# Kernel tuning notes

Measured on AMD Instinct MI355X. Metric: run time of the kernel, lower is better.

The kernel has to match this reference:

```python
import jax, jax.numpy as jnp
import numpy as np

N_NODES = 100000
N_EDGES = 3200000
D_IN = 128
D_OUT = 128


def setup_inputs() -> dict:
    key = jax.random.key(0)
    k1, k2, k3, k4, k5, k6 = jax.random.split(key, 6)
    x = jax.random.normal(k1, (N_NODES, D_IN), dtype=jnp.float32)
    edge_row = jnp.sort(jax.random.randint(k2, (N_EDGES,), 0, N_NODES, dtype=jnp.int32))
    edge_col = jax.random.randint(k3, (N_EDGES,), 0, N_NODES, dtype=jnp.int32)
    edge_val = jax.random.uniform(k4, (N_EDGES,), dtype=jnp.float32)
    stdv = 1.0 / np.sqrt(D_OUT)
    weight = jax.random.uniform(k5, (D_IN, D_OUT), dtype=jnp.float32, minval=-stdv, maxval=stdv)
    bias = jax.random.uniform(k6, (D_OUT,), dtype=jnp.float32, minval=-stdv, maxval=stdv)
    return {"x": x, "edge_row": edge_row, "edge_col": edge_col,
            "edge_val": edge_val, "weight": weight, "bias": bias}


def reference(x, edge_row, edge_col, edge_val, weight, bias):
    # support = A @ x  (sparse COO SpMM via gather + segment-sum scatter)
    gathered = x[edge_col] * edge_val[:, None]          # [E, D_IN]
    support = jax.ops.segment_sum(gathered, edge_row, num_segments=N_NODES)  # [N, D_IN]
    # output = support @ W + b
    return support @ weight + bias
```

## Files before the change

kernel.cpp:

```cpp
#include <hip/hip_runtime.h>

#define NNODES 100000
#define NEDGES 3200000
#define DIM    128

typedef __bf16  bf16x8 __attribute__((ext_vector_type(8)));
typedef unsigned short u16;
typedef u16     u16x8  __attribute__((ext_vector_type(8)));
typedef float   f32x4  __attribute__((ext_vector_type(4)));
typedef float   f32x2  __attribute__((ext_vector_type(2)));

__device__ __forceinline__ u16 f2bf(float f) {
    union { float f; unsigned int i; } c;
    c.f = f;
    unsigned int x = c.i;
    unsigned int rounding = 0x7fff + ((x >> 16) & 1);
    x += rounding;
    return (u16)(x >> 16);
}

__device__ __forceinline__ float bf2f(u16 u) {
    union { unsigned int i; float f; } c;
    c.i = ((unsigned int)u) << 16;
    return c.f;
}

__device__ __forceinline__ bf16x8 ldfrag_bf(const u16* p) {
    u16x8 u = *(const u16x8*)p;
    return __builtin_bit_cast(bf16x8, u);
}

__device__ __forceinline__ bf16x8 ldfrag_f32(const float* p) {
    f32x4 a = *(const f32x4*)p;
    f32x4 b = *(const f32x4*)(p + 4);
    u16x8 u;
#pragma unroll
    for (int i = 0; i < 4; ++i) u[i] = f2bf(a[i]);
#pragma unroll
    for (int i = 0; i < 4; ++i) u[4 + i] = f2bf(b[i]);
    return __builtin_bit_cast(bf16x8, u);
}

__global__ void build_row_ptr(const int* __restrict__ edge_row,
                              int* __restrict__ row_ptr) {
    int n = blockIdx.x * blockDim.x + threadIdx.x;
    if (n > NNODES) return;
    int lo = 0, hi = NEDGES;
    while (lo < hi) {
        int mid = (lo + hi) >> 1;
        if (edge_row[mid] < n) lo = mid + 1; else hi = mid;
    }
    row_ptr[n] = lo;
}

__global__ void prep_wt(const float* __restrict__ w, u16* __restrict__ wt) {
    int i = blockIdx.x * blockDim.x + threadIdx.x;
    if (i >= DIM * DIM) return;
    int k = i >> 7, n = i & 127;
    wt[n * DIM + k] = f2bf(w[k * DIM + n]);
}

__global__ __launch_bounds__(256) void gemm_xw(const float* __restrict__ x,
                                               const u16* __restrict__ wt,
                                               u16* __restrict__ y) {
    int wave = __builtin_amdgcn_readfirstlane(threadIdx.x >> 6);
    int lane = threadIdx.x & 63;
    int quad = lane >> 4, l16 = lane & 15;
    int mBase = (blockIdx.x * 4 + wave) * 16;
    if (mBase >= NNODES) return;

    const float* xrow = x + (size_t)(mBase + l16) * DIM + quad * 8;

    f32x4 acc[8];
#pragma unroll
    for (int nt = 0; nt < 8; ++nt) acc[nt] = (f32x4){0.f, 0.f, 0.f, 0.f};

#pragma unroll
    for (int kb = 0; kb < 4; ++kb) {
        bf16x8 a = ldfrag_f32(xrow + kb * 32);
#pragma unroll
        for (int nt = 0; nt < 8; ++nt) {
            bf16x8 b = ldfrag_bf(wt + (nt * 16 + l16) * DIM + kb * 32 + quad * 8);
            acc[nt] = __builtin_amdgcn_mfma_f32_16x16x32_bf16(a, b, acc[nt], 0, 0, 0);
        }
    }

#pragma unroll
    for (int nt = 0; nt < 8; ++nt) {
        int col = nt * 16 + l16;
#pragma unroll
        for (int r = 0; r < 4; ++r) {
            int row = mBase + quad * 4 + r;
            y[(size_t)row * DIM + col] = f2bf(acc[nt][r]);
        }
    }
}

__global__ __launch_bounds__(256) void spmm(const int* __restrict__ row_ptr,
                                            const int* __restrict__ ecol,
                                            const float* __restrict__ eval,
                                            const u16* __restrict__ y,
                                            const float* __restrict__ bias,
                                            float* __restrict__ out) {
    int wave = __builtin_amdgcn_readfirstlane(threadIdx.x >> 6);
    int lane = threadIdx.x & 63;
    int row  = blockIdx.x * 4 + wave;
    if (row >= NNODES) return;

    int lo = row_ptr[row];
    int hi = row_ptr[row + 1];

    float acc0 = bias[lane * 2];
    float acc1 = bias[lane * 2 + 1];

    int e = lo;
    for (; e + 4 <= hi; e += 4) {
        int   c0 = ecol[e],     c1 = ecol[e + 1];
        int   c2 = ecol[e + 2], c3 = ecol[e + 3];
        float v0 = eval[e],     v1 = eval[e + 1];
        float v2 = eval[e + 2], v3 = eval[e + 3];
        unsigned int p0 = *(const unsigned int*)(y + (size_t)c0 * DIM + lane * 2);
        unsigned int p1 = *(const unsigned int*)(y + (size_t)c1 * DIM + lane * 2);
        unsigned int p2 = *(const unsigned int*)(y + (size_t)c2 * DIM + lane * 2);
        unsigned int p3 = *(const unsigned int*)(y + (size_t)c3 * DIM + lane * 2);
        acc0 += v0 * bf2f((u16)(p0 & 0xffffu)) + v1 * bf2f((u16)(p1 & 0xffffu))
              + v2 * bf2f((u16)(p2 & 0xffffu)) + v3 * bf2f((u16)(p3 & 0xffffu));
        acc1 += v0 * bf2f((u16)(p0 >> 16))     + v1 * bf2f((u16)(p1 >> 16))
              + v2 * bf2f((u16)(p2 >> 16))     + v3 * bf2f((u16)(p3 >> 16));
    }
    for (; e < hi; ++e) {
        int   c0 = ecol[e];
        float v0 = eval[e];
        unsigned int p0 = *(const unsigned int*)(y + (size_t)c0 * DIM + lane * 2);
        acc0 += v0 * bf2f((u16)(p0 & 0xffffu));
        acc1 += v0 * bf2f((u16)(p0 >> 16));
    }

    f32x2 o; o[0] = acc0; o[1] = acc1;
    *(f32x2*)(out + (size_t)row * DIM + lane * 2) = o;
}

extern "C" void kernel_launch(void* const* d_in, const int* in_sizes, int n_in,
                              void* d_out, int out_size, void* d_ws, size_t ws_size,
                              hipStream_t stream) {
    const float* x        = (const float*)d_in[0];
    const int*   edge_row = (const int*)d_in[1];
    const int*   edge_col = (const int*)d_in[2];
    const float* edge_val = (const float*)d_in[3];
    const float* weight   = (const float*)d_in[4];
    const float* bias     = (const float*)d_in[5];
    float* out = (float*)d_out;

    char* ws = (char*)d_ws;
    u16* y       = (u16*)ws;
    int* row_ptr = (int*)(ws + (size_t)NNODES * DIM * 2);
    u16* wt      = (u16*)(ws + 26000128);

    prep_wt<<<(DIM * DIM + 255) / 256, 256, 0, stream>>>(weight, wt);
    build_row_ptr<<<(NNODES + 1 + 255) / 256, 256, 0, stream>>>(edge_row, row_ptr);

    gemm_xw<<<(NNODES / 16 + 3) / 4, 256, 0, stream>>>(x, wt, y);

    spmm<<<NNODES / 4, 256, 0, stream>>>(row_ptr, edge_col, edge_val, y, bias, out);
}
```

Measured before the change: 292.7 us.

## Stage weights in LDS for GEMM and split SpMM wave into two edge halves

```diff
diff --git a/kernel.cpp b/kernel.cpp
--- a/kernel.cpp
+++ b/kernel.cpp
@@ -8,7 +8,8 @@
 typedef unsigned short u16;
 typedef u16     u16x8  __attribute__((ext_vector_type(8)));
 typedef float   f32x4  __attribute__((ext_vector_type(4)));
-typedef float   f32x2  __attribute__((ext_vector_type(2)));
+typedef unsigned int u32;
+typedef u32     u32x2  __attribute__((ext_vector_type(2)));
 
 __device__ __forceinline__ u16 f2bf(float f) {
     union { float f; unsigned int i; } c;
@@ -25,7 +26,7 @@
     return c.f;
 }
 
-__device__ __forceinline__ bf16x8 ldfrag_bf(const u16* p) {
+__device__ __forceinline__ bf16x8 ldfrag_u16(const u16* p) {
     u16x8 u = *(const u16x8*)p;
     return __builtin_bit_cast(bf16x8, u);
 }
@@ -60,11 +61,26 @@
     wt[n * DIM + k] = f2bf(w[k * DIM + n]);
 }
 
+#define WT_STRIDE 136
 __global__ __launch_bounds__(256) void gemm_xw(const float* __restrict__ x,
                                                const u16* __restrict__ wt,
                                                u16* __restrict__ y) {
-    int wave = __builtin_amdgcn_readfirstlane(threadIdx.x >> 6);
-    int lane = threadIdx.x & 63;
+    __shared__ u16 wlds[DIM * WT_STRIDE];
+
+    int tid = threadIdx.x;
+    {
+        const f32x4* src = (const f32x4*)wt;
+#pragma unroll
+        for (int i = 0; i < 8; ++i) {
+            int ci  = tid + 256 * i;
+            int row = ci >> 4, off = ci & 15;
+            *((f32x4*)(wlds + row * WT_STRIDE) + off) = src[ci];
+        }
+    }
+    __syncthreads();
+
+    int wave = __builtin_amdgcn_readfirstlane(tid >> 6);
+    int lane = tid & 63;
     int quad = lane >> 4, l16 = lane & 15;
     int mBase = (blockIdx.x * 4 + wave) * 16;
     if (mBase >= NNODES) return;
@@ -80,7 +96,7 @@
         bf16x8 a = ldfrag_f32(xrow + kb * 32);
 #pragma unroll
         for (int nt = 0; nt < 8; ++nt) {
-            bf16x8 b = ldfrag_bf(wt + (nt * 16 + l16) * DIM + kb * 32 + quad * 8);
+            bf16x8 b = ldfrag_u16(wlds + (nt * 16 + l16) * WT_STRIDE + kb * 32 + quad * 8);
             acc[nt] = __builtin_amdgcn_mfma_f32_16x16x32_bf16(a, b, acc[nt], 0, 0, 0);
         }
     }
@@ -102,42 +118,71 @@
                                             const u16* __restrict__ y,
                                             const float* __restrict__ bias,
                                             float* __restrict__ out) {
-    int wave = __builtin_amdgcn_readfirstlane(threadIdx.x >> 6);
+    int wave = threadIdx.x >> 6;
     int lane = threadIdx.x & 63;
+    int half = lane >> 5;
+    int l32  = lane & 31;
     int row  = blockIdx.x * 4 + wave;
     if (row >= NNODES) return;
 
     int lo = row_ptr[row];
     int hi = row_ptr[row + 1];
 
-    float acc0 = bias[lane * 2];
-    float acc1 = bias[lane * 2 + 1];
+    float a0 = 0.f, a1 = 0.f, a2 = 0.f, a3 = 0.f;
+    const u16* yb = y + l32 * 4;
 
     int e = lo;
-    for (; e + 4 <= hi; e += 4) {
-        int   c0 = ecol[e],     c1 = ecol[e + 1];
-        int   c2 = ecol[e + 2], c3 = ecol[e + 3];
-        float v0 = eval[e],     v1 = eval[e + 1];
-        float v2 = eval[e + 2], v3 = eval[e + 3];
-        unsigned int p0 = *(const unsigned int*)(y + (size_t)c0 * DIM + lane * 2);
-        unsigned int p1 = *(const unsigned int*)(y + (size_t)c1 * DIM + lane * 2);
-        unsigned int p2 = *(const unsigned int*)(y + (size_t)c2 * DIM + lane * 2);
-        unsigned int p3 = *(const unsigned int*)(y + (size_t)c3 * DIM + lane * 2);
-        acc0 += v0 * bf2f((u16)(p0 & 0xffffu)) + v1 * bf2f((u16)(p1 & 0xffffu))
-              + v2 * bf2f((u16)(p2 & 0xffffu)) + v3 * bf2f((u16)(p3 & 0xffffu));
-        acc1 += v0 * bf2f((u16)(p0 >> 16))     + v1 * bf2f((u16)(p1 >> 16))
-              + v2 * bf2f((u16)(p2 >> 16))     + v3 * bf2f((u16)(p3 >> 16));
-    }
-    for (; e < hi; ++e) {
-        int   c0 = ecol[e];
-        float v0 = eval[e];
-        unsigned int p0 = *(const unsigned int*)(y + (size_t)c0 * DIM + lane * 2);
-        acc0 += v0 * bf2f((u16)(p0 & 0xffffu));
-        acc1 += v0 * bf2f((u16)(p0 >> 16));
-    }
-
-    f32x2 o; o[0] = acc0; o[1] = acc1;
-    *(f32x2*)(out + (size_t)row * DIM + lane * 2) = o;
+    for (; e + 8 <= hi; e += 8) {
+        int c[4]; float v[4];
+#pragma unroll
+        for (int s = 0; s < 4; ++s) {
+            c[s] = __builtin_nontemporal_load(ecol + e + 2 * s + half);
+            v[s] = __builtin_nontemporal_load(eval + e + 2 * s + half);
+        }
+        u32x2 p[4];
+#pragma unroll
+        for (int s = 0; s < 4; ++s)
+            p[s] = *(const u32x2*)(yb + (size_t)c[s] * DIM);
+#pragma unroll
+        for (int s = 0; s < 4; ++s) {
+            a0 += v[s] * bf2f((u16)(p[s][0] & 0xffffu));
+            a1 += v[s] * bf2f((u16)(p[s][0] >> 16));
+            a2 += v[s] * bf2f((u16)(p[s][1] & 0xffffu));
+            a3 += v[s] * bf2f((u16)(p[s][1] >> 16));
+        }
+    }
+    for (; e + 2 <= hi; e += 2) {
+        int   c = __builtin_nontemporal_load(ecol + e + half);
+        float v = __builtin_nontemporal_load(eval + e + half);
+        u32x2 p = *(const u32x2*)(yb + (size_t)c * DIM);
+        a0 += v * bf2f((u16)(p[0] & 0xffffu));
+        a1 += v * bf2f((u16)(p[0] >> 16));
+        a2 += v * bf2f((u16)(p[1] & 0xffffu));
+        a3 += v * bf2f((u16)(p[1] >> 16));
+    }
+    if (e < hi && half == 0) {
+        int   c = ecol[e];
+        float v = eval[e];
+        u32x2 p = *(const u32x2*)(yb + (size_t)c * DIM);
+        a0 += v * bf2f((u16)(p[0] & 0xffffu));
+        a1 += v * bf2f((u16)(p[0] >> 16));
+        a2 += v * bf2f((u16)(p[1] & 0xffffu));
+        a3 += v * bf2f((u16)(p[1] >> 16));
+    }
+
+    a0 += __shfl_xor(a0, 32);
+    a1 += __shfl_xor(a1, 32);
+    a2 += __shfl_xor(a2, 32);
+    a3 += __shfl_xor(a3, 32);
+
+    if (half == 0) {
+        f32x4 o;
+        o[0] = a0 + bias[l32 * 4 + 0];
+        o[1] = a1 + bias[l32 * 4 + 1];
+        o[2] = a2 + bias[l32 * 4 + 2];
+        o[3] = a3 + bias[l32 * 4 + 3];
+        __builtin_nontemporal_store(o, (f32x4*)(out + (size_t)row * DIM + l32 * 4));
+    }
 }
 
 extern "C" void kernel_launch(void* const* d_in, const int* in_sizes, int n_in,
```

Measured after the change: 276.6 us. 1.06x faster.
